# Kernel tuning notes

Measured on AMD Instinct MI355X. Metric: run time of the kernel, lower is better.

## Reference

```python
import jax, jax.numpy as jnp
import numpy as np
from jax import lax

EPS = 1e-6

def _ls_scale_weights(max_scale):
    # Least-squares slope coefficients of log(measure) vs log(window size):
    # alpha = sum_r c_r * log(mu_r), c_r = (l_r - mean(l)) / sum((l - mean(l))^2)
    l = np.log(np.array([2.0 * r + 1.0 for r in range(1, max_scale + 1)], dtype=np.float32))
    c = (l - l.mean()) / np.sum((l - l.mean()) ** 2)
    return jnp.asarray(c, dtype=jnp.float32)

def setup_inputs() -> dict:
    key = jax.random.key(0)
    k1, k2, k3 = jax.random.split(key, 3)
    B, H, W, C = 16, 112, 112, 64
    MAX_SCALE, K = 4, 8
    x = jax.random.normal(k1, (B, H, W, C), dtype=jnp.float32)
    scale_weights = _ls_scale_weights(MAX_SCALE)
    # per-channel histogram anchors (centers) and positive widths
    centers = jax.random.normal(k2, (C, K), dtype=jnp.float32)
    widths = jax.random.uniform(k3, (C, K), dtype=jnp.float32, minval=0.1, maxval=1.0)
    return {"x": x, "scale_weights": scale_weights, "centers": centers, "widths": widths}

def _forward(x, scale_weights, centers, widths):
    max_scale = scale_weights.shape[0]
    xa = jnp.abs(x) + EPS  # nonnegative local measure
    # multiscale box measures mu_r via SAME sum-pooling over (2r+1)x(2r+1) windows
    log_mus = []
    for r in range(1, max_scale + 1):
        w = 2 * r + 1
        mu = lax.reduce_window(xa, 0.0, lax.add, (1, w, w, 1), (1, 1, 1, 1), 'SAME')
        log_mus.append(jnp.log(mu))
    logs = jnp.stack(log_mus, axis=0)  # [S, B, H, W, C]
    alphas = jnp.einsum('s,sbhwc->bhwc', scale_weights, logs)  # [B, H, W, C]
    # soft L2 histogram: per-channel anchors, membership 1 - width * (alpha - center)^2
    d = alphas[..., None] - centers  # [B, H, W, C, K]
    hist = 1.0 - widths * (d * d)
    soft_counts = jnp.sum(jax.nn.relu(hist), axis=-1)  # [B, H, W, C]
    return x + jax.nn.sigmoid(soft_counts)

def reference(x, scale_weights, centers, widths):
    return _forward(x, scale_weights, centers, widths)
```

## Files before the change

### kernel.cpp

```cpp
#include <hip/hip_runtime.h>
#include <math.h>

#define BB   16
#define HH   112
#define WW   112
#define CC   64
#define KK   8
#define EPSF 1e-6f
#define LN2F 0.69314718055994530942f

#define WPT  7
#define HPT  2
#define NR   10

typedef float v2f __attribute__((ext_vector_type(2)));

template<bool HE, bool WE, int I0, int NC>
__device__ __forceinline__ void process_chunk(const float* __restrict__ x,
                                              const int* rowoff,
                                              const float* rvalid,
                                              int w0, int c, int voff0,
                                              v2f* mu1, v2f* mu2, v2f* mu3, v2f* mu4,
                                              float* arawA, float* arawB)
{
    float a[NC][NR];
    if constexpr (!WE) {
#pragma unroll
        for (int j = 0; j < NC; ++j) {
            const int co = voff0 + (I0 + j) * CC;
#pragma unroll
            for (int dh = 0; dh < NR; ++dh)
                a[j][dh] = x[rowoff[dh] + co];
        }
    } else {
        int coloff[NC];
#pragma unroll
        for (int j = 0; j < NC; ++j) {
            const int wc  = w0 - 4 + I0 + j;
            const int wcc = min(max(wc, 0), WW - 1);
            coloff[j] = wcc * CC + c;
        }
#pragma unroll
        for (int j = 0; j < NC; ++j)
#pragma unroll
            for (int dh = 0; dh < NR; ++dh)
                a[j][dh] = x[rowoff[dh] + coloff[j]];
    }

#pragma unroll
    for (int j = 0; j < NC; ++j) {
        const int i = I0 + j;
        if (i >= 4 && i <= 10) { arawA[i - 4] = a[j][4]; arawB[i - 4] = a[j][5]; }
    }

#pragma unroll
    for (int j = 0; j < NC; ++j) {
        const int i = I0 + j;
        float v0 = fabsf(a[j][0]);
        float v1 = fabsf(a[j][1]);
        float v2 = fabsf(a[j][2]);
        float v3 = fabsf(a[j][3]);
        float v4 = fabsf(a[j][4]);
        float v5 = fabsf(a[j][5]);
        float v6 = fabsf(a[j][6]);
        float v7 = fabsf(a[j][7]);
        float v8 = fabsf(a[j][8]);
        float v9 = fabsf(a[j][9]);
        if (HE) {
            v0 *= rvalid[0]; v1 *= rvalid[1]; v2 *= rvalid[2]; v3 *= rvalid[3];
            v4 *= rvalid[4]; v5 *= rvalid[5]; v6 *= rvalid[6]; v7 *= rvalid[7];
            v8 *= rvalid[8]; v9 *= rvalid[9];
        }
        const float tA1 = v3 + v4 + v5;
        const float tA2 = tA1 + v2 + v6;
        const float tA3 = tA2 + v1 + v7;
        const float tA4 = tA3 + v0 + v8;
        v2f t1 = { tA1, tA1 + (v6 - v3) };
        v2f t2 = { tA2, tA2 + (v7 - v2) };
        v2f t3 = { tA3, tA3 + (v8 - v1) };
        v2f t4 = { tA4, tA4 + (v9 - v0) };
        if (WE) {
            const bool ok = (unsigned)(w0 - 4 + i) < (unsigned)WW;
            const float m = ok ? 1.0f : 0.0f;
            t1 *= m; t2 *= m; t3 *= m; t4 *= m;
        }
#pragma unroll
        for (int wi = 0; wi < WPT; ++wi) {
            const int ci = wi + 4;
            if (i >= ci - 1 && i <= ci + 1) mu1[wi] += t1;
            if (i >= ci - 2 && i <= ci + 2) mu2[wi] += t2;
            if (i >= ci - 3 && i <= ci + 3) mu3[wi] += t3;
            if (i >= ci - 4 && i <= ci + 4) mu4[wi] += t4;
        }
    }
}

template<bool HE, bool WE>
__device__ __forceinline__ void do_tile(const float* __restrict__ x,
                                        float* __restrict__ out,
                                        int b, int h0, int w0, int c,
                                        float s1, float s2, float s3, float s4,
                                        const float* cen, const float* wid)
{
    int rowoff[NR];
    float rvalid[NR];
#pragma unroll
    for (int dh = 0; dh < NR; ++dh) {
        const int hr = h0 + dh - 4;
        const int hc = HE ? min(max(hr, 0), HH - 1) : hr;
        rowoff[dh] = (b * HH + hc) * WW * CC;
        rvalid[dh] = HE ? (((unsigned)hr < (unsigned)HH) ? 1.0f : 0.0f) : 1.0f;
    }

    const int voff0 = (w0 - 4) * CC + c;

    v2f mu1[WPT], mu2[WPT], mu3[WPT], mu4[WPT];
    float arawA[WPT], arawB[WPT];
#pragma unroll
    for (int i = 0; i < WPT; ++i) {
        mu1[i] = (v2f)0.0f; mu2[i] = (v2f)0.0f;
        mu3[i] = (v2f)0.0f; mu4[i] = (v2f)0.0f;
    }

    process_chunk<HE, WE, 0,  5>(x, rowoff, rvalid, w0, c, voff0, mu1, mu2, mu3, mu4, arawA, arawB);
    process_chunk<HE, WE, 5,  5>(x, rowoff, rvalid, w0, c, voff0, mu1, mu2, mu3, mu4, arawA, arawB);
    process_chunk<HE, WE, 10, 5>(x, rowoff, rvalid, w0, c, voff0, mu1, mu2, mu3, mu4, arawA, arawB);

    v2f r1 = {3.f, 3.f}, r2 = {5.f, 5.f}, r3 = {7.f, 7.f}, r4 = {9.f, 9.f};
    if (HE) {
        const int gA = h0, gB = h0 + 1;
        r1 = (v2f){ (float)(min(gA+1,HH-1)-max(gA-1,0)+1), (float)(min(gB+1,HH-1)-max(gB-1,0)+1) };
        r2 = (v2f){ (float)(min(gA+2,HH-1)-max(gA-2,0)+1), (float)(min(gB+2,HH-1)-max(gB-2,0)+1) };
        r3 = (v2f){ (float)(min(gA+3,HH-1)-max(gA-3,0)+1), (float)(min(gB+3,HH-1)-max(gB-3,0)+1) };
        r4 = (v2f){ (float)(min(gA+4,HH-1)-max(gA-4,0)+1), (float)(min(gB+4,HH-1)-max(gB-4,0)+1) };
    }

    float* __restrict__ orowA = out + rowoff[4];
    float* __restrict__ orowB = out + rowoff[5];
    const int voffC = w0 * CC + c;
    const v2f zero = (v2f)0.0f;

#pragma unroll
    for (int wi = 0; wi < WPT; ++wi) {
        float c1 = 3.f, c2 = 5.f, c3 = 7.f, c4 = 9.f;
        if (WE) {
            const int w = w0 + wi;
            c1 = (float)(min(w + 1, WW - 1) - max(w - 1, 0) + 1);
            c2 = (float)(min(w + 2, WW - 1) - max(w - 2, 0) + 1);
            c3 = (float)(min(w + 3, WW - 1) - max(w - 3, 0) + 1);
            c4 = (float)(min(w + 4, WW - 1) - max(w - 4, 0) + 1);
        }
        const v2f m1 = mu1[wi] + r1 * (c1 * EPSF);
        const v2f m2 = mu2[wi] + r2 * (c2 * EPSF);
        const v2f m3 = mu3[wi] + r3 * (c3 * EPSF);
        const v2f m4 = mu4[wi] + r4 * (c4 * EPSF);

        const v2f l1 = { __log2f(m1.x), __log2f(m1.y) };
        const v2f l2 = { __log2f(m2.x), __log2f(m2.y) };
        const v2f l3 = { __log2f(m3.x), __log2f(m3.y) };
        const v2f l4 = { __log2f(m4.x), __log2f(m4.y) };

        const v2f alpha = l1 * s1 + l2 * s2 + l3 * s3 + l4 * s4;

        v2f sc = zero;
#pragma unroll
        for (int k = 0; k < KK; ++k) {
            const v2f d  = alpha - cen[k];
            const v2f hv = 1.0f - wid[k] * (d * d);
            sc += __builtin_elementwise_max(hv, zero);
        }

        const float sigA = __fdividef(1.0f, 1.0f + __expf(-sc.x));
        const float sigB = __fdividef(1.0f, 1.0f + __expf(-sc.y));
        orowA[voffC + wi * CC] = arawA[wi] + sigA;
        orowB[voffC + wi * CC] = arawB[wi] + sigB;
    }
}

__global__ __launch_bounds__(256, 3)
void l2hist_singularity_kernel(const float* __restrict__ x,
                               const float* __restrict__ sw,
                               const float* __restrict__ centers,
                               const float* __restrict__ widths,
                               float* __restrict__ out)
{
    const int tid = threadIdx.x;
    const int c   = tid & 63;
    const int wq  = tid >> 6;

    const int blk = blockIdx.x;
    const int wt  = blk & 3;
    const int ht  = (blk >> 2) % (HH / HPT);
    const int b   = (blk >> 2) / (HH / HPT);
    const int h0  = ht * HPT;
    const int w0  = wt * 28 + wq * WPT;

    const float s1 = sw[0] * LN2F, s2 = sw[1] * LN2F;
    const float s3 = sw[2] * LN2F, s4 = sw[3] * LN2F;

    float cen[KK], wid[KK];
#pragma unroll
    for (int k = 0; k < KK; ++k) {
        cen[k] = centers[c * KK + k];
        wid[k] = widths[c * KK + k];
    }

    const bool he = (h0 < 4) | (h0 + HPT - 1 + 4 >= HH);
    const bool we = (w0 < 4) | (w0 + WPT - 1 + 4 >= WW);

    if (!he) {
        if (!we) do_tile<false, false>(x, out, b, h0, w0, c, s1, s2, s3, s4, cen, wid);
        else     do_tile<false, true >(x, out, b, h0, w0, c, s1, s2, s3, s4, cen, wid);
    } else {
        if (!we) do_tile<true,  false>(x, out, b, h0, w0, c, s1, s2, s3, s4, cen, wid);
        else     do_tile<true,  true >(x, out, b, h0, w0, c, s1, s2, s3, s4, cen, wid);
    }
}

extern "C" void kernel_launch(void* const* d_in, const int* in_sizes, int n_in,
                              void* d_out, int out_size, void* d_ws, size_t ws_size,
                              hipStream_t stream) {
    const float* x       = (const float*)d_in[0];
    const float* sw      = (const float*)d_in[1];
    const float* centers = (const float*)d_in[2];
    const float* widths  = (const float*)d_in[3];
    float* out           = (float*)d_out;

    const int blocks = BB * (HH / HPT) * (WW / 28);
    l2hist_singularity_kernel<<<blocks, 256, 0, stream>>>(x, sw, centers, widths, out);
}
```

Measured before the change: 49.10 us.

## Remap threads to channel pairs with float2 loads and one row per wave

```diff
diff --git a/kernel.cpp b/kernel.cpp
--- a/kernel.cpp
+++ b/kernel.cpp
@@ -10,8 +10,7 @@
 #define LN2F 0.69314718055994530942f
 
 #define WPT  7
-#define HPT  2
-#define NR   10
+#define NRR  9
 
 typedef float v2f __attribute__((ext_vector_type(2)));
 
@@ -19,68 +18,56 @@
 __device__ __forceinline__ void process_chunk(const float* __restrict__ x,
                                               const int* rowoff,
                                               const float* rvalid,
-                                              int w0, int c, int voff0,
-                                              v2f* mu1, v2f* mu2, v2f* mu3, v2f* mu4,
-                                              float* arawA, float* arawB)
+                                              int w0l, int c0, int voff0,
+                                              v2f* mu1, v2f* mu2, v2f* mu3, v2f* mu4)
 {
-    float a[NC][NR];
+    v2f q[NC][NRR];
     if constexpr (!WE) {
 #pragma unroll
         for (int j = 0; j < NC; ++j) {
             const int co = voff0 + (I0 + j) * CC;
 #pragma unroll
-            for (int dh = 0; dh < NR; ++dh)
-                a[j][dh] = x[rowoff[dh] + co];
+            for (int dh = 0; dh < NRR; ++dh)
+                q[j][dh] = *(const v2f*)(x + rowoff[dh] + co);
         }
     } else {
         int coloff[NC];
 #pragma unroll
         for (int j = 0; j < NC; ++j) {
-            const int wc  = w0 - 4 + I0 + j;
+            const int wc  = w0l - 4 + I0 + j;
             const int wcc = min(max(wc, 0), WW - 1);
-            coloff[j] = wcc * CC + c;
+            coloff[j] = wcc * CC + c0;
         }
 #pragma unroll
         for (int j = 0; j < NC; ++j)
 #pragma unroll
-            for (int dh = 0; dh < NR; ++dh)
-                a[j][dh] = x[rowoff[dh] + coloff[j]];
+            for (int dh = 0; dh < NRR; ++dh)
+                q[j][dh] = *(const v2f*)(x + rowoff[dh] + coloff[j]);
     }
 
 #pragma unroll
     for (int j = 0; j < NC; ++j) {
         const int i = I0 + j;
-        if (i >= 4 && i <= 10) { arawA[i - 4] = a[j][4]; arawB[i - 4] = a[j][5]; }
-    }
-
-#pragma unroll
-    for (int j = 0; j < NC; ++j) {
-        const int i = I0 + j;
-        float v0 = fabsf(a[j][0]);
-        float v1 = fabsf(a[j][1]);
-        float v2 = fabsf(a[j][2]);
-        float v3 = fabsf(a[j][3]);
-        float v4 = fabsf(a[j][4]);
-        float v5 = fabsf(a[j][5]);
-        float v6 = fabsf(a[j][6]);
-        float v7 = fabsf(a[j][7]);
-        float v8 = fabsf(a[j][8]);
-        float v9 = fabsf(a[j][9]);
+        v2f a0 = __builtin_elementwise_abs(q[j][0]);
+        v2f a1 = __builtin_elementwise_abs(q[j][1]);
+        v2f a2 = __builtin_elementwise_abs(q[j][2]);
+        v2f a3 = __builtin_elementwise_abs(q[j][3]);
+        v2f a4 = __builtin_elementwise_abs(q[j][4]);
+        v2f a5 = __builtin_elementwise_abs(q[j][5]);
+        v2f a6 = __builtin_elementwise_abs(q[j][6]);
+        v2f a7 = __builtin_elementwise_abs(q[j][7]);
+        v2f a8 = __builtin_elementwise_abs(q[j][8]);
         if (HE) {
-            v0 *= rvalid[0]; v1 *= rvalid[1]; v2 *= rvalid[2]; v3 *= rvalid[3];
-            v4 *= rvalid[4]; v5 *= rvalid[5]; v6 *= rvalid[6]; v7 *= rvalid[7];
-            v8 *= rvalid[8]; v9 *= rvalid[9];
-        }
-        const float tA1 = v3 + v4 + v5;
-        const float tA2 = tA1 + v2 + v6;
-        const float tA3 = tA2 + v1 + v7;
-        const float tA4 = tA3 + v0 + v8;
-        v2f t1 = { tA1, tA1 + (v6 - v3) };
-        v2f t2 = { tA2, tA2 + (v7 - v2) };
-        v2f t3 = { tA3, tA3 + (v8 - v1) };
-        v2f t4 = { tA4, tA4 + (v9 - v0) };
+            a0 *= rvalid[0]; a1 *= rvalid[1]; a2 *= rvalid[2]; a3 *= rvalid[3];
+            a4 *= rvalid[4]; a5 *= rvalid[5]; a6 *= rvalid[6]; a7 *= rvalid[7];
+            a8 *= rvalid[8];
+        }
+        v2f t1 = a3 + a4 + a5;
+        v2f t2 = t1 + a2 + a6;
+        v2f t3 = t2 + a1 + a7;
+        v2f t4 = t3 + a0 + a8;
         if (WE) {
-            const bool ok = (unsigned)(w0 - 4 + i) < (unsigned)WW;
+            const bool ok = (unsigned)(w0l - 4 + i) < (unsigned)WW;
             const float m = ok ? 1.0f : 0.0f;
             t1 *= m; t2 *= m; t3 *= m; t4 *= m;
         }
@@ -98,62 +85,70 @@
 template<bool HE, bool WE>
 __device__ __forceinline__ void do_tile(const float* __restrict__ x,
                                         float* __restrict__ out,
-                                        int b, int h0, int w0, int c,
-                                        float s1, float s2, float s3, float s4,
-                                        const float* cen, const float* wid)
+                                        const float* __restrict__ centers,
+                                        const float* __restrict__ widths,
+                                        int b, int h, int w0l, int c0,
+                                        float s1, float s2, float s3, float s4)
 {
-    int rowoff[NR];
-    float rvalid[NR];
-#pragma unroll
-    for (int dh = 0; dh < NR; ++dh) {
-        const int hr = h0 + dh - 4;
+    int rowoff[NRR];
+    float rvalid[NRR];
+#pragma unroll
+    for (int dh = 0; dh < NRR; ++dh) {
+        const int hr = h + dh - 4;
         const int hc = HE ? min(max(hr, 0), HH - 1) : hr;
         rowoff[dh] = (b * HH + hc) * WW * CC;
         rvalid[dh] = HE ? (((unsigned)hr < (unsigned)HH) ? 1.0f : 0.0f) : 1.0f;
     }
 
-    const int voff0 = (w0 - 4) * CC + c;
+    const int voff0 = (w0l - 4) * CC + c0;
 
     v2f mu1[WPT], mu2[WPT], mu3[WPT], mu4[WPT];
-    float arawA[WPT], arawB[WPT];
 #pragma unroll
     for (int i = 0; i < WPT; ++i) {
         mu1[i] = (v2f)0.0f; mu2[i] = (v2f)0.0f;
         mu3[i] = (v2f)0.0f; mu4[i] = (v2f)0.0f;
     }
 
-    process_chunk<HE, WE, 0,  5>(x, rowoff, rvalid, w0, c, voff0, mu1, mu2, mu3, mu4, arawA, arawB);
-    process_chunk<HE, WE, 5,  5>(x, rowoff, rvalid, w0, c, voff0, mu1, mu2, mu3, mu4, arawA, arawB);
-    process_chunk<HE, WE, 10, 5>(x, rowoff, rvalid, w0, c, voff0, mu1, mu2, mu3, mu4, arawA, arawB);
-
-    v2f r1 = {3.f, 3.f}, r2 = {5.f, 5.f}, r3 = {7.f, 7.f}, r4 = {9.f, 9.f};
+    process_chunk<HE, WE, 0,  3>(x, rowoff, rvalid, w0l, c0, voff0, mu1, mu2, mu3, mu4);
+    process_chunk<HE, WE, 3,  3>(x, rowoff, rvalid, w0l, c0, voff0, mu1, mu2, mu3, mu4);
+    process_chunk<HE, WE, 6,  3>(x, rowoff, rvalid, w0l, c0, voff0, mu1, mu2, mu3, mu4);
+    process_chunk<HE, WE, 9,  3>(x, rowoff, rvalid, w0l, c0, voff0, mu1, mu2, mu3, mu4);
+    process_chunk<HE, WE, 12, 3>(x, rowoff, rvalid, w0l, c0, voff0, mu1, mu2, mu3, mu4);
+
+    v2f cen[KK], nwid[KK];
+#pragma unroll
+    for (int k = 0; k < KK; ++k) {
+        cen[k]  = (v2f){  centers[c0 * KK + k],  centers[c0 * KK + KK + k] };
+        nwid[k] = (v2f){ -widths[c0 * KK + k],  -widths[c0 * KK + KK + k] };
+    }
+
+    int rows1 = 3, rows2 = 5, rows3 = 7, rows4 = 9;
     if (HE) {
-        const int gA = h0, gB = h0 + 1;
-        r1 = (v2f){ (float)(min(gA+1,HH-1)-max(gA-1,0)+1), (float)(min(gB+1,HH-1)-max(gB-1,0)+1) };
-        r2 = (v2f){ (float)(min(gA+2,HH-1)-max(gA-2,0)+1), (float)(min(gB+2,HH-1)-max(gB-2,0)+1) };
-        r3 = (v2f){ (float)(min(gA+3,HH-1)-max(gA-3,0)+1), (float)(min(gB+3,HH-1)-max(gB-3,0)+1) };
-        r4 = (v2f){ (float)(min(gA+4,HH-1)-max(gA-4,0)+1), (float)(min(gB+4,HH-1)-max(gB-4,0)+1) };
-    }
-
-    float* __restrict__ orowA = out + rowoff[4];
-    float* __restrict__ orowB = out + rowoff[5];
-    const int voffC = w0 * CC + c;
+        rows1 = min(h + 1, HH - 1) - max(h - 1, 0) + 1;
+        rows2 = min(h + 2, HH - 1) - max(h - 2, 0) + 1;
+        rows3 = min(h + 3, HH - 1) - max(h - 3, 0) + 1;
+        rows4 = min(h + 4, HH - 1) - max(h - 4, 0) + 1;
+    }
+
+    const float* __restrict__ xrow = x  + rowoff[4];
+    float* __restrict__       orow = out + rowoff[4];
+    const int voffC = w0l * CC + c0;
     const v2f zero = (v2f)0.0f;
 
 #pragma unroll
     for (int wi = 0; wi < WPT; ++wi) {
         float c1 = 3.f, c2 = 5.f, c3 = 7.f, c4 = 9.f;
         if (WE) {
-            const int w = w0 + wi;
+            const int w = w0l + wi;
             c1 = (float)(min(w + 1, WW - 1) - max(w - 1, 0) + 1);
             c2 = (float)(min(w + 2, WW - 1) - max(w - 2, 0) + 1);
             c3 = (float)(min(w + 3, WW - 1) - max(w - 3, 0) + 1);
             c4 = (float)(min(w + 4, WW - 1) - max(w - 4, 0) + 1);
         }
-        const v2f m1 = mu1[wi] + r1 * (c1 * EPSF);
-        const v2f m2 = mu2[wi] + r2 * (c2 * EPSF);
-        const v2f m3 = mu3[wi] + r3 * (c3 * EPSF);
-        const v2f m4 = mu4[wi] + r4 * (c4 * EPSF);
+        const v2f m1 = mu1[wi] + (float)rows1 * c1 * EPSF;
+        const v2f m2 = mu2[wi] + (float)rows2 * c2 * EPSF;
+        const v2f m3 = mu3[wi] + (float)rows3 * c3 * EPSF;
+        const v2f m4 = mu4[wi] + (float)rows4 * c4 * EPSF;
 
         const v2f l1 = { __log2f(m1.x), __log2f(m1.y) };
         const v2f l2 = { __log2f(m2.x), __log2f(m2.y) };
@@ -166,14 +161,15 @@
 #pragma unroll
         for (int k = 0; k < KK; ++k) {
             const v2f d  = alpha - cen[k];
-            const v2f hv = 1.0f - wid[k] * (d * d);
+            const v2f hv = nwid[k] * (d * d) + 1.0f;
             sc += __builtin_elementwise_max(hv, zero);
         }
 
-        const float sigA = __fdividef(1.0f, 1.0f + __expf(-sc.x));
-        const float sigB = __fdividef(1.0f, 1.0f + __expf(-sc.y));
-        orowA[voffC + wi * CC] = arawA[wi] + sigA;
-        orowB[voffC + wi * CC] = arawB[wi] + sigB;
+        const v2f xv = *(const v2f*)(xrow + voffC + wi * CC);
+        v2f o;
+        o.x = xv.x + __fdividef(1.0f, 1.0f + __expf(-sc.x));
+        o.y = xv.y + __fdividef(1.0f, 1.0f + __expf(-sc.y));
+        *(v2f*)(orow + voffC + wi * CC) = o;
     }
 }
 
@@ -184,36 +180,33 @@
                                const float* __restrict__ widths,
                                float* __restrict__ out)
 {
-    const int tid = threadIdx.x;
-    const int c   = tid & 63;
-    const int wq  = tid >> 6;
-
-    const int blk = blockIdx.x;
-    const int wt  = blk & 3;
-    const int ht  = (blk >> 2) % (HH / HPT);
-    const int b   = (blk >> 2) / (HH / HPT);
-    const int h0  = ht * HPT;
-    const int w0  = wt * 28 + wq * WPT;
+    const int tid  = threadIdx.x;
+    const int wid  = __builtin_amdgcn_readfirstlane(tid >> 6);
+    const int lane = tid & 63;
+    const int cp   = lane & 31;
+    const int wsub = lane >> 5;
+    const int c0   = cp * 2;
+
+    int blk = blockIdx.x;
+    const int wt = blk & 3;
+    const int ht = (blk >> 2) % (HH / 2);
+    const int b  = (blk >> 2) / (HH / 2);
+    const int h   = ht * 2 + (wid >> 1);
+    const int w0w = wt * 28 + (wid & 1) * 14;
+    const int w0l = w0w + wsub * WPT;
 
     const float s1 = sw[0] * LN2F, s2 = sw[1] * LN2F;
     const float s3 = sw[2] * LN2F, s4 = sw[3] * LN2F;
 
-    float cen[KK], wid[KK];
-#pragma unroll
-    for (int k = 0; k < KK; ++k) {
-        cen[k] = centers[c * KK + k];
-        wid[k] = widths[c * KK + k];
-    }
-
-    const bool he = (h0 < 4) | (h0 + HPT - 1 + 4 >= HH);
-    const bool we = (w0 < 4) | (w0 + WPT - 1 + 4 >= WW);
+    const bool he = (ht < 2) | (ht >= (HH / 2) - 2);
+    const bool we = (w0w < 4) | (w0w + 13 + 4 >= WW);
 
     if (!he) {
-        if (!we) do_tile<false, false>(x, out, b, h0, w0, c, s1, s2, s3, s4, cen, wid);
-        else     do_tile<false, true >(x, out, b, h0, w0, c, s1, s2, s3, s4, cen, wid);
+        if (!we) do_tile<false, false>(x, out, centers, widths, b, h, w0l, c0, s1, s2, s3, s4);
+        else     do_tile<false, true >(x, out, centers, widths, b, h, w0l, c0, s1, s2, s3, s4);
     } else {
-        if (!we) do_tile<true,  false>(x, out, b, h0, w0, c, s1, s2, s3, s4, cen, wid);
-        else     do_tile<true,  true >(x, out, b, h0, w0, c, s1, s2, s3, s4, cen, wid);
+        if (!we) do_tile<true,  false>(x, out, centers, widths, b, h, w0l, c0, s1, s2, s3, s4);
+        else     do_tile<true,  true >(x, out, centers, widths, b, h, w0l, c0, s1, s2, s3, s4);
     }
 }
 
@@ -226,6 +219,6 @@
     const float* widths  = (const float*)d_in[3];
     float* out           = (float*)d_out;
 
-    const int blocks = BB * (HH / HPT) * (WW / 28);
+    const int blocks = BB * (HH / 2) * (WW / 28);
     l2hist_singularity_kernel<<<blocks, 256, 0, stream>>>(x, sw, centers, widths, out);
 }
```

After: 74.92 us. 1.53x slower.
